# Kernel optimization log

Hardware: AMD Instinct MI355X
Metric: run time of the kernel (lower is better)

Reference implementation:

```python
import jax, jax.numpy as jnp
import numpy as np

N = 8192

def setup_inputs() -> dict:
    key = jax.random.key(0)
    adj = jax.random.uniform(key, (N, N), dtype=jnp.float32)  # nonnegative weights
    return {"adj": adj}

def reference(adj) -> jnp.ndarray:
    # Symmetrize: adj + adj_T*(adj_T>adj) - adj*(adj_T>adj) == elementwise max(adj, adj^T)
    a = jnp.maximum(adj, adj.T)
    # Add self-loops: set diagonal to exactly 1 (adj + diag(1 - diag_part(adj)))
    n = a.shape[0]
    eye = jnp.eye(n, dtype=jnp.bool_)
    a = jnp.where(eye, jnp.ones((), a.dtype), a)
    # D^{-1/2} A D^{-1/2}: diag matmuls are equivalent to row/col scaling (O(n^2))
    d_inv_sqrt = jax.lax.rsqrt(jnp.sum(a, axis=1))  # [N]
    return a * d_inv_sqrt[:, None] * d_inv_sqrt[None, :]
```

## Files before the change

kernel.cpp:

```cpp
#include <hip/hip_runtime.h>

#define N 8192
#define T 64
#define TILES (N / T)
#define NPAIRS (TILES * (TILES + 1) / 2)
#define LDS_STRIDE 65
#define BLOCK 512

__device__ inline void decode_pair(int p, int& bi, int& bj) {
    float t = (float)TILES + 0.5f;
    int g = (int)(t - sqrtf(t * t - 2.0f * (float)p));
    if (g < 0) g = 0;
    if (g > TILES - 1) g = TILES - 1;
    while (g < TILES - 1 && ((g + 1) * TILES - (g + 1) * g / 2) <= p) g++;
    while (g > 0 && (g * TILES - g * (g - 1) / 2) > p) g--;
    bi = g;
    bj = bi + (p - (bi * TILES - bi * (bi - 1) / 2));
}

__device__ inline void load_tile(const float* __restrict__ src, int row0, int col0,
                                 float* lds) {
    int t = threadIdx.x;
    int c4 = t & 15;
    int r0 = t >> 4;
    #pragma unroll
    for (int rr = r0; rr < T; rr += 32) {
        const float4 v = *(const float4*)(src + (size_t)(row0 + rr) * N + col0 + c4 * 4);
        float* d = lds + rr * LDS_STRIDE + c4 * 4;
        d[0] = v.x; d[1] = v.y; d[2] = v.z; d[3] = v.w;
    }
}

__global__ __launch_bounds__(BLOCK) void k_rowsum(const float* __restrict__ adj,
                                                  float* __restrict__ rowsum) {
    __shared__ float ldsA[T * LDS_STRIDE];
    __shared__ float ldsB[T * LDS_STRIDE];
    __shared__ float red[BLOCK];
    int bi, bj;
    decode_pair((int)blockIdx.x, bi, bj);

    load_tile(adj, bi * T, bj * T, ldsA);
    load_tile(adj, bj * T, bi * T, ldsB);
    __syncthreads();

    int t = threadIdx.x;
    int lane = t & 63;
    int w = t >> 6;

    float acc = 0.0f;
    #pragma unroll
    for (int k = 0; k < 8; k++) {
        int c = w * 8 + k;
        float m = fmaxf(ldsA[lane * LDS_STRIDE + c], ldsB[c * LDS_STRIDE + lane]);
        if (bi == bj && lane == c) m = 1.0f;
        acc += m;
    }
    red[t] = acc;
    __syncthreads();
    if (t < 64) {
        float s = 0.0f;
        #pragma unroll
        for (int w2 = 0; w2 < 8; w2++) s += red[w2 * 64 + t];
        atomicAdd(&rowsum[bi * T + t], s);
    }

    if (bi != bj) {
        __syncthreads();
        float acc2 = 0.0f;
        #pragma unroll
        for (int k = 0; k < 8; k++) {
            int r = w * 8 + k;
            acc2 += fmaxf(ldsA[r * LDS_STRIDE + lane], ldsB[lane * LDS_STRIDE + r]);
        }
        red[t] = acc2;
        __syncthreads();
        if (t < 64) {
            float s = 0.0f;
            #pragma unroll
            for (int w2 = 0; w2 < 8; w2++) s += red[w2 * 64 + t];
            atomicAdd(&rowsum[bj * T + t], s);
        }
    }
}

__global__ __launch_bounds__(BLOCK) void k_scale(const float* __restrict__ adj,
                                                 const float* __restrict__ rowsum,
                                                 float* __restrict__ out) {
    __shared__ float ldsA[T * LDS_STRIDE];
    __shared__ float ldsB[T * LDS_STRIDE];
    __shared__ float dinvA[T];
    __shared__ float dinvB[T];
    int bi, bj;
    decode_pair((int)blockIdx.x, bi, bj);

    int t = threadIdx.x;
    if (t < 64)       dinvA[t]      = rsqrtf(rowsum[bi * T + t]);
    else if (t < 128) dinvB[t - 64] = rsqrtf(rowsum[bj * T + (t - 64)]);
    load_tile(adj, bi * T, bj * T, ldsA);
    load_tile(adj, bj * T, bi * T, ldsB);
    __syncthreads();

    int c4 = t & 15;
    int r0 = t >> 4;
    #pragma unroll
    for (int rr = r0; rr < T; rr += 32) {
        float4 v;
        float* vp = &v.x;
        #pragma unroll
        for (int k = 0; k < 4; k++) {
            int cc = c4 * 4 + k;
            float m = fmaxf(ldsA[rr * LDS_STRIDE + cc], ldsB[cc * LDS_STRIDE + rr]);
            if (bi == bj && rr == cc) m = 1.0f;
            vp[k] = m * dinvA[rr] * dinvB[cc];
        }
        *(float4*)(out + (size_t)(bi * T + rr) * N + bj * T + c4 * 4) = v;
    }
    if (bi != bj) {
        #pragma unroll
        for (int rr = r0; rr < T; rr += 32) {
            float4 v;
            float* vp = &v.x;
            #pragma unroll
            for (int k = 0; k < 4; k++) {
                int cc = c4 * 4 + k;
                float m = fmaxf(ldsB[rr * LDS_STRIDE + cc], ldsA[cc * LDS_STRIDE + rr]);
                vp[k] = m * dinvB[rr] * dinvA[cc];
            }
            *(float4*)(out + (size_t)(bj * T + rr) * N + bi * T + c4 * 4) = v;
        }
    }
}

extern "C" void kernel_launch(void* const* d_in, const int* in_sizes, int n_in,
                              void* d_out, int out_size, void* d_ws, size_t ws_size,
                              hipStream_t stream) {
    const float* adj = (const float*)d_in[0];
    float* out = (float*)d_out;
    float* rowsum = (float*)d_ws;

    hipMemsetAsync(rowsum, 0, N * sizeof(float), stream);
    k_rowsum<<<NPAIRS, BLOCK, 0, stream>>>(adj, rowsum);
    k_scale<<<NPAIRS, BLOCK, 0, stream>>>(adj, rowsum, out);
}
```

Before: 499.8 us.

## Process four tile pairs per block with register prefetch and nontemporal stores

Each block now handles four tile pairs grouped by super-tiles, so the grid shrinks from 8256 blocks to 2064. While the current pair is computed from LDS, the next pair's tiles are prefetched into registers. Row-sum contributions for a shared bi are accumulated across pairs before a single atomic flush, and output writes use nontemporal stores. The aim is to hide global load latency, reduce atomics and block-launch overhead, and avoid polluting the cache with output, at the cost of more complex decoding and extra barriers.

```diff
diff --git a/kernel.cpp b/kernel.cpp
--- a/kernel.cpp
+++ b/kernel.cpp
@@ -3,31 +3,45 @@
 #define N 8192
 #define T 64
 #define TILES (N / T)
-#define NPAIRS (TILES * (TILES + 1) / 2)
+#define SUP 8
+#define NSUP (TILES / SUP)
+#define PPB 4
+#define NBLOCKS 2064
 #define LDS_STRIDE 65
 #define BLOCK 512
 
-__device__ inline void decode_pair(int p, int& bi, int& bj) {
-    float t = (float)TILES + 0.5f;
-    int g = (int)(t - sqrtf(t * t - 2.0f * (float)p));
-    if (g < 0) g = 0;
-    if (g > TILES - 1) g = TILES - 1;
-    while (g < TILES - 1 && ((g + 1) * TILES - (g + 1) * g / 2) <= p) g++;
-    while (g > 0 && (g * TILES - g * (g - 1) / 2) > p) g--;
-    bi = g;
-    bj = bi + (p - (bi * TILES - bi * (bi - 1) / 2));
-}
-
-__device__ inline void load_tile(const float* __restrict__ src, int row0, int col0,
-                                 float* lds) {
-    int t = threadIdx.x;
-    int c4 = t & 15;
-    int r0 = t >> 4;
-    #pragma unroll
-    for (int rr = r0; rr < T; rr += 32) {
-        const float4 v = *(const float4*)(src + (size_t)(row0 + rr) * N + col0 + c4 * 4);
-        float* d = lds + rr * LDS_STRIDE + c4 * 4;
-        d[0] = v.x; d[1] = v.y; d[2] = v.z; d[3] = v.w;
+typedef float nfloat4 __attribute__((ext_vector_type(4)));
+
+__device__ inline void decode_block(int b, int bis[PPB], int bjs[PPB]) {
+    int BI = 0;
+    #pragma unroll 1
+    while (BI < NSUP - 1) {
+        int nb = BI + 1;
+        if (257 * nb - 8 * nb * nb <= b) BI = nb; else break;
+    }
+    int rem = b - (257 * BI - 8 * BI * BI);
+    if (rem < 9) {
+        #pragma unroll
+        for (int u = 0; u < PPB; u++) {
+            int l = 4 * rem + u;
+            int i = 0;
+            #pragma unroll 1
+            while ((i + 1) * 8 - (i + 1) * i / 2 <= l) i++;
+            int j = i + (l - (i * 8 - i * (i - 1) / 2));
+            bis[u] = BI * SUP + i;
+            bjs[u] = BI * SUP + j;
+        }
+    } else {
+        int r2 = rem - 9;
+        int d = (r2 >> 4) + 1;
+        int q = r2 & 15;
+        int i = q >> 1;
+        int j0 = (q & 1) * 4;
+        #pragma unroll
+        for (int u = 0; u < PPB; u++) {
+            bis[u] = BI * SUP + i;
+            bjs[u] = (BI + d) * SUP + j0 + u;
+        }
     }
 }
 
@@ -36,49 +50,86 @@
     __shared__ float ldsA[T * LDS_STRIDE];
     __shared__ float ldsB[T * LDS_STRIDE];
     __shared__ float red[BLOCK];
-    int bi, bj;
-    decode_pair((int)blockIdx.x, bi, bj);
-
-    load_tile(adj, bi * T, bj * T, ldsA);
-    load_tile(adj, bj * T, bi * T, ldsB);
-    __syncthreads();
+    int bis[PPB], bjs[PPB];
+    decode_block((int)blockIdx.x, bis, bjs);
 
     int t = threadIdx.x;
+    int c4 = t & 15;
+    int r0 = t >> 4;
     int lane = t & 63;
     int w = t >> 6;
 
-    float acc = 0.0f;
+    float4 nA0, nA1, nB0, nB1;
+    {
+        const float* pa = adj + (size_t)(bis[0] * T + r0) * N + bjs[0] * T + c4 * 4;
+        nA0 = *(const float4*)pa;
+        nA1 = *(const float4*)(pa + (size_t)32 * N);
+        const float* pb = adj + (size_t)(bjs[0] * T + r0) * N + bis[0] * T + c4 * 4;
+        nB0 = *(const float4*)pb;
+        nB1 = *(const float4*)(pb + (size_t)32 * N);
+    }
+
+    float accA = 0.0f;
     #pragma unroll
-    for (int k = 0; k < 8; k++) {
-        int c = w * 8 + k;
-        float m = fmaxf(ldsA[lane * LDS_STRIDE + c], ldsB[c * LDS_STRIDE + lane]);
-        if (bi == bj && lane == c) m = 1.0f;
-        acc += m;
-    }
-    red[t] = acc;
-    __syncthreads();
-    if (t < 64) {
-        float s = 0.0f;
-        #pragma unroll
-        for (int w2 = 0; w2 < 8; w2++) s += red[w2 * 64 + t];
-        atomicAdd(&rowsum[bi * T + t], s);
-    }
-
-    if (bi != bj) {
+    for (int k = 0; k < PPB; k++) {
+        int bi = bis[k], bj = bjs[k];
+        if (k > 0) __syncthreads();
+        {
+            float* d0 = ldsA + r0 * LDS_STRIDE + c4 * 4;
+            d0[0] = nA0.x; d0[1] = nA0.y; d0[2] = nA0.z; d0[3] = nA0.w;
+            float* d1 = ldsA + (r0 + 32) * LDS_STRIDE + c4 * 4;
+            d1[0] = nA1.x; d1[1] = nA1.y; d1[2] = nA1.z; d1[3] = nA1.w;
+            float* e0 = ldsB + r0 * LDS_STRIDE + c4 * 4;
+            e0[0] = nB0.x; e0[1] = nB0.y; e0[2] = nB0.z; e0[3] = nB0.w;
+            float* e1 = ldsB + (r0 + 32) * LDS_STRIDE + c4 * 4;
+            e1[0] = nB1.x; e1[1] = nB1.y; e1[2] = nB1.z; e1[3] = nB1.w;
+        }
+        if (k + 1 < PPB) {
+            const float* pa = adj + (size_t)(bis[k + 1] * T + r0) * N + bjs[k + 1] * T + c4 * 4;
+            nA0 = *(const float4*)pa;
+            nA1 = *(const float4*)(pa + (size_t)32 * N);
+            const float* pb = adj + (size_t)(bjs[k + 1] * T + r0) * N + bis[k + 1] * T + c4 * 4;
+            nB0 = *(const float4*)pb;
+            nB1 = *(const float4*)(pb + (size_t)32 * N);
+        }
         __syncthreads();
-        float acc2 = 0.0f;
-        #pragma unroll
-        for (int k = 0; k < 8; k++) {
-            int r = w * 8 + k;
-            acc2 += fmaxf(ldsA[r * LDS_STRIDE + lane], ldsB[lane * LDS_STRIDE + r]);
-        }
-        red[t] = acc2;
-        __syncthreads();
-        if (t < 64) {
-            float s = 0.0f;
+
+        if (bi != bj) {
+            float acc2 = 0.0f;
             #pragma unroll
-            for (int w2 = 0; w2 < 8; w2++) s += red[w2 * 64 + t];
-            atomicAdd(&rowsum[bj * T + t], s);
+            for (int kk = 0; kk < 8; kk++) {
+                int r = w * 8 + kk;
+                acc2 += fmaxf(ldsA[r * LDS_STRIDE + lane], ldsB[lane * LDS_STRIDE + r]);
+            }
+            red[t] = acc2;
+            __syncthreads();
+            if (t < 64) {
+                float s = 0.0f;
+                #pragma unroll
+                for (int w2 = 0; w2 < 8; w2++) s += red[w2 * 64 + t];
+                atomicAdd(&rowsum[bj * T + t], s);
+            }
+        }
+
+        #pragma unroll
+        for (int kk = 0; kk < 8; kk++) {
+            int c = w * 8 + kk;
+            float m = fmaxf(ldsA[lane * LDS_STRIDE + c], ldsB[c * LDS_STRIDE + lane]);
+            if (bi == bj && lane == c) m = 1.0f;
+            accA += m;
+        }
+        bool flush = (k == PPB - 1) || (bis[k + 1] != bi);
+        if (flush) {
+            __syncthreads();
+            red[t] = accA;
+            __syncthreads();
+            if (t < 64) {
+                float s = 0.0f;
+                #pragma unroll
+                for (int w2 = 0; w2 < 8; w2++) s += red[w2 * 64 + t];
+                atomicAdd(&rowsum[bi * T + t], s);
+            }
+            accA = 0.0f;
         }
     }
 }
@@ -88,45 +139,82 @@
                                                  float* __restrict__ out) {
     __shared__ float ldsA[T * LDS_STRIDE];
     __shared__ float ldsB[T * LDS_STRIDE];
-    __shared__ float dinvA[T];
-    __shared__ float dinvB[T];
-    int bi, bj;
-    decode_pair((int)blockIdx.x, bi, bj);
+    __shared__ float dA[T];
+    __shared__ float dB[T];
+    int bis[PPB], bjs[PPB];
+    decode_block((int)blockIdx.x, bis, bjs);
 
     int t = threadIdx.x;
-    if (t < 64)       dinvA[t]      = rsqrtf(rowsum[bi * T + t]);
-    else if (t < 128) dinvB[t - 64] = rsqrtf(rowsum[bj * T + (t - 64)]);
-    load_tile(adj, bi * T, bj * T, ldsA);
-    load_tile(adj, bj * T, bi * T, ldsB);
-    __syncthreads();
-
     int c4 = t & 15;
     int r0 = t >> 4;
+
+    float rA[PPB], rB[PPB];
     #pragma unroll
-    for (int rr = r0; rr < T; rr += 32) {
-        float4 v;
-        float* vp = &v.x;
-        #pragma unroll
-        for (int k = 0; k < 4; k++) {
-            int cc = c4 * 4 + k;
-            float m = fmaxf(ldsA[rr * LDS_STRIDE + cc], ldsB[cc * LDS_STRIDE + rr]);
-            if (bi == bj && rr == cc) m = 1.0f;
-            vp[k] = m * dinvA[rr] * dinvB[cc];
-        }
-        *(float4*)(out + (size_t)(bi * T + rr) * N + bj * T + c4 * 4) = v;
-    }
-    if (bi != bj) {
+    for (int u = 0; u < PPB; u++) {
+        if (t < 64)       rA[u] = rowsum[bis[u] * T + t];
+        else if (t < 128) rB[u] = rowsum[bjs[u] * T + (t - 64)];
+    }
+
+    float4 nA0, nA1, nB0, nB1;
+    {
+        const float* pa = adj + (size_t)(bis[0] * T + r0) * N + bjs[0] * T + c4 * 4;
+        nA0 = *(const float4*)pa;
+        nA1 = *(const float4*)(pa + (size_t)32 * N);
+        const float* pb = adj + (size_t)(bjs[0] * T + r0) * N + bis[0] * T + c4 * 4;
+        nB0 = *(const float4*)pb;
+        nB1 = *(const float4*)(pb + (size_t)32 * N);
+    }
+
+    #pragma unroll
+    for (int k = 0; k < PPB; k++) {
+        int bi = bis[k], bj = bjs[k];
+        if (k > 0) __syncthreads();
+        {
+            float* d0 = ldsA + r0 * LDS_STRIDE + c4 * 4;
+            d0[0] = nA0.x; d0[1] = nA0.y; d0[2] = nA0.z; d0[3] = nA0.w;
+            float* d1 = ldsA + (r0 + 32) * LDS_STRIDE + c4 * 4;
+            d1[0] = nA1.x; d1[1] = nA1.y; d1[2] = nA1.z; d1[3] = nA1.w;
+            float* e0 = ldsB + r0 * LDS_STRIDE + c4 * 4;
+            e0[0] = nB0.x; e0[1] = nB0.y; e0[2] = nB0.z; e0[3] = nB0.w;
+            float* e1 = ldsB + (r0 + 32) * LDS_STRIDE + c4 * 4;
+            e1[0] = nB1.x; e1[1] = nB1.y; e1[2] = nB1.z; e1[3] = nB1.w;
+        }
+        if (t < 64)       dA[t]      = rsqrtf(rA[k]);
+        else if (t < 128) dB[t - 64] = rsqrtf(rB[k]);
+        if (k + 1 < PPB) {
+            const float* pa = adj + (size_t)(bis[k + 1] * T + r0) * N + bjs[k + 1] * T + c4 * 4;
+            nA0 = *(const float4*)pa;
+            nA1 = *(const float4*)(pa + (size_t)32 * N);
+            const float* pb = adj + (size_t)(bjs[k + 1] * T + r0) * N + bis[k + 1] * T + c4 * 4;
+            nB0 = *(const float4*)pb;
+            nB1 = *(const float4*)(pb + (size_t)32 * N);
+        }
+        __syncthreads();
+
         #pragma unroll
         for (int rr = r0; rr < T; rr += 32) {
-            float4 v;
-            float* vp = &v.x;
+            nfloat4 v;
             #pragma unroll
-            for (int k = 0; k < 4; k++) {
-                int cc = c4 * 4 + k;
-                float m = fmaxf(ldsB[rr * LDS_STRIDE + cc], ldsA[cc * LDS_STRIDE + rr]);
-                vp[k] = m * dinvB[rr] * dinvA[cc];
-            }
-            *(float4*)(out + (size_t)(bj * T + rr) * N + bi * T + c4 * 4) = v;
+            for (int kk = 0; kk < 4; kk++) {
+                int cc = c4 * 4 + kk;
+                float m = fmaxf(ldsA[rr * LDS_STRIDE + cc], ldsB[cc * LDS_STRIDE + rr]);
+                if (bi == bj && rr == cc) m = 1.0f;
+                v[kk] = m * dA[rr] * dB[cc];
+            }
+            __builtin_nontemporal_store(v, (nfloat4*)(out + (size_t)(bi * T + rr) * N + bj * T + c4 * 4));
+        }
+        if (bi != bj) {
+            #pragma unroll
+            for (int rr = r0; rr < T; rr += 32) {
+                nfloat4 v;
+                #pragma unroll
+                for (int kk = 0; kk < 4; kk++) {
+                    int cc = c4 * 4 + kk;
+                    float m = fmaxf(ldsB[rr * LDS_STRIDE + cc], ldsA[cc * LDS_STRIDE + rr]);
+                    v[kk] = m * dB[rr] * dA[cc];
+                }
+                __builtin_nontemporal_store(v, (nfloat4*)(out + (size_t)(bj * T + rr) * N + bi * T + c4 * 4));
+            }
         }
     }
 }
@@ -138,7 +226,7 @@
     float* out = (float*)d_out;
     float* rowsum = (float*)d_ws;
 
-    hipMemsetAsync(rowsum, 0, N * sizeof(float), stream);
-    k_rowsum<<<NPAIRS, BLOCK, 0, stream>>>(adj, rowsum);
-    k_scale<<<NPAIRS, BLOCK, 0, stream>>>(adj, rowsum, out);
-}
+    (void)hipMemsetAsync(rowsum, 0, N * sizeof(float), stream);
+    k_rowsum<<<NBLOCKS, BLOCK, 0, stream>>>(adj, rowsum);
+    k_scale<<<NBLOCKS, BLOCK, 0, stream>>>(adj, rowsum, out);
+}
```

Result: faster. 488.9 us (-2.2%).

## Replace LDS tile transpose with per-thread 4x4 register micro-tiles

Applied to the files above, without the earlier changes.

Both kernels now have each thread load a 4x4 block of the tile and the matching 4x4 block of the transposed tile straight into registers. The thread forms max(a, a^T) locally, so the LDS staging buffers and their barrier are gone. Row sums are reduced with wavefront shuffles, and column sums go through a small padded LDS array. Block size drops to 256. In exchange, the global loads of the transposed block are 16-byte reads spread over 16 rows, which may coalesce less well than the earlier row-contiguous tile loads.

```diff
diff --git a/kernel.cpp b/kernel.cpp
--- a/kernel.cpp
+++ b/kernel.cpp
@@ -4,8 +4,7 @@
 #define T 64
 #define TILES (N / T)
 #define NPAIRS (TILES * (TILES + 1) / 2)
-#define LDS_STRIDE 65
-#define BLOCK 512
+#define BLOCK 256
 
 __device__ inline void decode_pair(int p, int& bi, int& bj) {
     float t = (float)TILES + 0.5f;
@@ -15,69 +14,57 @@
     while (g < TILES - 1 && ((g + 1) * TILES - (g + 1) * g / 2) <= p) g++;
     while (g > 0 && (g * TILES - g * (g - 1) / 2) > p) g--;
     bi = g;
-    bj = bi + (p - (bi * TILES - bi * (bi - 1) / 2));
+    bj = g + (p - (g * TILES - g * (g - 1) / 2));
 }
 
-__device__ inline void load_tile(const float* __restrict__ src, int row0, int col0,
-                                 float* lds) {
-    int t = threadIdx.x;
-    int c4 = t & 15;
-    int r0 = t >> 4;
-    #pragma unroll
-    for (int rr = r0; rr < T; rr += 32) {
-        const float4 v = *(const float4*)(src + (size_t)(row0 + rr) * N + col0 + c4 * 4);
-        float* d = lds + rr * LDS_STRIDE + c4 * 4;
-        d[0] = v.x; d[1] = v.y; d[2] = v.z; d[3] = v.w;
-    }
-}
 
 __global__ __launch_bounds__(BLOCK) void k_rowsum(const float* __restrict__ adj,
                                                   float* __restrict__ rowsum) {
-    __shared__ float ldsA[T * LDS_STRIDE];
-    __shared__ float ldsB[T * LDS_STRIDE];
-    __shared__ float red[BLOCK];
+    __shared__ float red[T * 17];
     int bi, bj;
     decode_pair((int)blockIdx.x, bi, bj);
+    bool diag = (bi == bj);
+    int t = threadIdx.x;
+    int c4 = t & 15, r4 = t >> 4;
 
-    load_tile(adj, bi * T, bj * T, ldsA);
-    load_tile(adj, bj * T, bi * T, ldsB);
-    __syncthreads();
+    float4 va[4], vb[4];
+    const float* pa = adj + (size_t)(bi * T + 4 * r4) * N + bj * T + 4 * c4;
+    #pragma unroll
+    for (int x = 0; x < 4; x++) va[x] = *(const float4*)(pa + (size_t)x * N);
+    const float* pb = adj + (size_t)(bj * T + 4 * c4) * N + bi * T + 4 * r4;
+    #pragma unroll
+    for (int y = 0; y < 4; y++) vb[y] = *(const float4*)(pb + (size_t)y * N);
 
-    int t = threadIdx.x;
-    int lane = t & 63;
-    int w = t >> 6;
-
-    float acc = 0.0f;
+    float rowP[4] = {0.f, 0.f, 0.f, 0.f};
+    float colP[4] = {0.f, 0.f, 0.f, 0.f};
     #pragma unroll
-    for (int k = 0; k < 8; k++) {
-        int c = w * 8 + k;
-        float m = fmaxf(ldsA[lane * LDS_STRIDE + c], ldsB[c * LDS_STRIDE + lane]);
-        if (bi == bj && lane == c) m = 1.0f;
-        acc += m;
-    }
-    red[t] = acc;
-    __syncthreads();
-    if (t < 64) {
-        float s = 0.0f;
+    for (int x = 0; x < 4; x++) {
+        const float* ax = (const float*)&va[x];
         #pragma unroll
-        for (int w2 = 0; w2 < 8; w2++) s += red[w2 * 64 + t];
-        atomicAdd(&rowsum[bi * T + t], s);
+        for (int y = 0; y < 4; y++) {
+            float b = ((const float*)&vb[y])[x];
+            float m = fmaxf(ax[y], b);
+            if (diag && (4 * r4 + x == 4 * c4 + y)) m = 1.0f;
+            rowP[x] += m;
+            colP[y] += m;
+        }
     }
 
-    if (bi != bj) {
-        __syncthreads();
-        float acc2 = 0.0f;
+    #pragma unroll
+    for (int mask = 1; mask <= 8; mask <<= 1) {
         #pragma unroll
-        for (int k = 0; k < 8; k++) {
-            int r = w * 8 + k;
-            acc2 += fmaxf(ldsA[r * LDS_STRIDE + lane], ldsB[lane * LDS_STRIDE + r]);
-        }
-        red[t] = acc2;
+        for (int x = 0; x < 4; x++) rowP[x] += __shfl_xor(rowP[x], mask);
+    }
+    if (c4 < 4) atomicAdd(&rowsum[bi * T + 4 * r4 + c4], rowP[c4]);
+
+    if (!diag) {
+        #pragma unroll
+        for (int y = 0; y < 4; y++) red[(4 * c4 + y) * 17 + r4] = colP[y];
         __syncthreads();
         if (t < 64) {
-            float s = 0.0f;
+            float s = 0.f;
             #pragma unroll
-            for (int w2 = 0; w2 < 8; w2++) s += red[w2 * 64 + t];
+            for (int k = 0; k < 16; k++) s += red[t * 17 + k];
             atomicAdd(&rowsum[bj * T + t], s);
         }
     }
@@ -86,47 +73,59 @@
 __global__ __launch_bounds__(BLOCK) void k_scale(const float* __restrict__ adj,
                                                  const float* __restrict__ rowsum,
                                                  float* __restrict__ out) {
-    __shared__ float ldsA[T * LDS_STRIDE];
-    __shared__ float ldsB[T * LDS_STRIDE];
-    __shared__ float dinvA[T];
-    __shared__ float dinvB[T];
     int bi, bj;
     decode_pair((int)blockIdx.x, bi, bj);
+    bool diag = (bi == bj);
+    int t = threadIdx.x;
+    int c4 = t & 15, r4 = t >> 4;
 
-    int t = threadIdx.x;
-    if (t < 64)       dinvA[t]      = rsqrtf(rowsum[bi * T + t]);
-    else if (t < 128) dinvB[t - 64] = rsqrtf(rowsum[bj * T + (t - 64)]);
-    load_tile(adj, bi * T, bj * T, ldsA);
-    load_tile(adj, bj * T, bi * T, ldsB);
-    __syncthreads();
+    float4 va[4], vb[4];
+    const float* pa = adj + (size_t)(bi * T + 4 * r4) * N + bj * T + 4 * c4;
+    #pragma unroll
+    for (int x = 0; x < 4; x++) va[x] = *(const float4*)(pa + (size_t)x * N);
+    const float* pb = adj + (size_t)(bj * T + 4 * c4) * N + bi * T + 4 * r4;
+    #pragma unroll
+    for (int y = 0; y < 4; y++) vb[y] = *(const float4*)(pb + (size_t)y * N);
 
-    int c4 = t & 15;
-    int r0 = t >> 4;
+    float dA[4], dB[4];
     #pragma unroll
-    for (int rr = r0; rr < T; rr += 32) {
+    for (int x = 0; x < 4; x++) dA[x] = rsqrtf(rowsum[bi * T + 4 * r4 + x]);
+    #pragma unroll
+    for (int y = 0; y < 4; y++) dB[y] = rsqrtf(rowsum[bj * T + 4 * c4 + y]);
+
+    float m[4][4];
+    #pragma unroll
+    for (int x = 0; x < 4; x++) {
+        const float* ax = (const float*)&va[x];
+        #pragma unroll
+        for (int y = 0; y < 4; y++) {
+            float b = ((const float*)&vb[y])[x];
+            float v = fmaxf(ax[y], b);
+            if (diag && (4 * r4 + x == 4 * c4 + y)) v = 1.0f;
+            m[x][y] = v;
+        }
+    }
+
+    float* po = out + (size_t)(bi * T + 4 * r4) * N + bj * T + 4 * c4;
+    #pragma unroll
+    for (int x = 0; x < 4; x++) {
         float4 v;
-        float* vp = &v.x;
+        v.x = m[x][0] * dA[x] * dB[0];
+        v.y = m[x][1] * dA[x] * dB[1];
+        v.z = m[x][2] * dA[x] * dB[2];
+        v.w = m[x][3] * dA[x] * dB[3];
+        *(float4*)(po + (size_t)x * N) = v;
+    }
+    if (!diag) {
+        float* pm = out + (size_t)(bj * T + 4 * c4) * N + bi * T + 4 * r4;
         #pragma unroll
-        for (int k = 0; k < 4; k++) {
-            int cc = c4 * 4 + k;
-            float m = fmaxf(ldsA[rr * LDS_STRIDE + cc], ldsB[cc * LDS_STRIDE + rr]);
-            if (bi == bj && rr == cc) m = 1.0f;
-            vp[k] = m * dinvA[rr] * dinvB[cc];
-        }
-        *(float4*)(out + (size_t)(bi * T + rr) * N + bj * T + c4 * 4) = v;
-    }
-    if (bi != bj) {
-        #pragma unroll
-        for (int rr = r0; rr < T; rr += 32) {
-            float4 v;
-            float* vp = &v.x;
-            #pragma unroll
-            for (int k = 0; k < 4; k++) {
-                int cc = c4 * 4 + k;
-                float m = fmaxf(ldsB[rr * LDS_STRIDE + cc], ldsA[cc * LDS_STRIDE + rr]);
-                vp[k] = m * dinvB[rr] * dinvA[cc];
-            }
-            *(float4*)(out + (size_t)(bj * T + rr) * N + bi * T + c4 * 4) = v;
+        for (int y = 0; y < 4; y++) {
+            float4 u;
+            u.x = m[0][y] * dB[y] * dA[0];
+            u.y = m[1][y] * dB[y] * dA[1];
+            u.z = m[2][y] * dB[y] * dA[2];
+            u.w = m[3][y] * dB[y] * dA[3];
+            *(float4*)(pm + (size_t)y * N) = u;
         }
     }
 }
@@ -138,7 +137,7 @@
     float* out = (float*)d_out;
     float* rowsum = (float*)d_ws;
 
-    hipMemsetAsync(rowsum, 0, N * sizeof(float), stream);
+    (void)hipMemsetAsync(rowsum, 0, N * sizeof(float), stream);
     k_rowsum<<<NPAIRS, BLOCK, 0, stream>>>(adj, rowsum);
     k_scale<<<NPAIRS, BLOCK, 0, stream>>>(adj, rowsum, out);
 }
```

Result: no change. 507.6 us (+1.6%).
